# Optimization experiments

Hardware: AMD Instinct MI355X
Metric: run time of the kernel (lower is better)

The kernel has to match this reference:

```python
import jax, jax.numpy as jnp
import numpy as np

NUM_TOKENS = 16384
HIDDEN = 4096
NUM_EXPERTS = 256
TOP_K = 8
N_GROUP = 8
TOPK_GROUP = 4
NORM_TOPK_PROB = True
ROUTED_SCALING_FACTOR = 1.0


def setup_inputs() -> dict:
    key = jax.random.key(0)
    k1, k2, k3 = jax.random.split(key, 3)
    hidden_states = jax.random.normal(k1, (NUM_TOKENS, HIDDEN), dtype=jnp.float32)
    weight = jax.random.normal(k2, (NUM_EXPERTS, HIDDEN), dtype=jnp.float32) * (HIDDEN ** -0.5)
    e_score_correction_bias = jax.random.normal(k3, (NUM_EXPERTS,), dtype=jnp.float32) * 0.01
    return {"hidden_states": hidden_states, "weight": weight,
            "e_score_correction_bias": e_score_correction_bias}


def reference(hidden_states, weight, e_score_correction_bias):
    num_tokens = hidden_states.shape[0]
    # router logits: [T, E]
    logits = jnp.einsum('th,eh->te', hidden_states.astype(jnp.float32),
                        weight.astype(jnp.float32))
    scores = jax.nn.sigmoid(logits)
    scores_for_choice = scores + e_score_correction_bias[None, :]
    # group scores: sum of top-2 within each group, [T, G]
    per_group = scores_for_choice.reshape(num_tokens, N_GROUP, NUM_EXPERTS // N_GROUP)
    top2_vals, _ = jax.lax.top_k(per_group, 2)
    group_scores = top2_vals.sum(axis=-1)
    # select topk_group groups, build mask over experts
    _, group_idx = jax.lax.top_k(group_scores, TOPK_GROUP)  # [T, topk_group]
    group_mask = jnp.zeros_like(group_scores).at[
        jnp.arange(num_tokens)[:, None], group_idx].set(1.0)  # [T, G]
    score_mask = jnp.repeat(group_mask, NUM_EXPERTS // N_GROUP, axis=1)  # [T, E]
    tmp_scores = jnp.where(score_mask > 0, scores_for_choice, -jnp.inf)
    # final top-k experts over masked scores
    _, topk_idx = jax.lax.top_k(tmp_scores, TOP_K)  # [T, K]
    topk_weight = jnp.take_along_axis(scores, topk_idx, axis=1)
    if TOP_K > 1 and NORM_TOPK_PROB:
        denom = topk_weight.sum(axis=-1, keepdims=True) + 1e-20
        topk_weight = topk_weight / denom
    topk_weight = topk_weight * ROUTED_SCALING_FACTOR
    return logits, topk_weight, topk_idx
```

## Files before the change

kernel.cpp:

```cpp
#include <hip/hip_runtime.h>
#include <hip/hip_bf16.h>
#include <math.h>

#define TKN 16384
#define HID 4096
#define NE  256
#define TOPK 8
#define NGRP 8
#define TOPG 4

#define BM 64
#define BK 64
#define NKT (HID / BK)
#define BIMG 16384

typedef _Float16 half8 __attribute__((ext_vector_type(8)));
typedef float    f32x4 __attribute__((ext_vector_type(4)));

static __device__ __forceinline__ unsigned pkrtz(float x, float y) {
    auto r = __builtin_amdgcn_cvt_pkrtz(x, y);
    return __builtin_bit_cast(unsigned, r);
}
static __device__ __forceinline__ float hi_mask(float a) {
    return __uint_as_float(__float_as_uint(a) & 0xFFFFE000u);
}
static __device__ __forceinline__ void gload_lds16(const void* g, void* l) {
    __builtin_amdgcn_global_load_lds(
        (const __attribute__((address_space(1))) unsigned int*)g,
        (__attribute__((address_space(3))) unsigned int*)l, 16, 0, 0);
}

__global__ __launch_bounds__(256) void prep_b(const float* __restrict__ B,
                                              unsigned char* __restrict__ ws)
{
    const int gid = blockIdx.x * 256 + threadIdx.x;
    const int e   = gid >> 9;
    const int k0  = (gid & 511) * 8;
    const float* src = B + (size_t)e * HID + k0;
    float v[8];
    #pragma unroll
    for (int i = 0; i < 8; ++i) v[i] = src[i];
    unsigned hw[4], lw[4];
    #pragma unroll
    for (int j = 0; j < 4; ++j) {
        const float x0 = v[2*j], x1 = v[2*j+1];
        const float h0 = hi_mask(x0), h1 = hi_mask(x1);
        hw[j] = pkrtz(h0, h1);
        lw[j] = pkrtz(x0 - h0, x1 - h1);
    }
    const int cb     = e >> 6;
    const int colgrp = (e & 63) >> 4;
    const int lane16 = e & 15;
    const int kt     = k0 >> 6;
    const int kk     = k0 & 63;
    const int wg     = kk >> 5;
    const int kseg   = (kk >> 3) & 3;
    const int f      = colgrp * 2 + wg;
    unsigned char* img = ws + (size_t)(cb * NKT + kt) * BIMG
                            + f * 2048 + (kseg * 16 + lane16) * 16;
    *(uint4*)(img)        = make_uint4(hw[0], hw[1], hw[2], hw[3]);
    *(uint4*)(img + 1024) = make_uint4(lw[0], lw[1], lw[2], lw[3]);
}

__global__ __launch_bounds__(256, 4) void gemm_mfma(
    const float* __restrict__ A, const unsigned char* __restrict__ Bws,
    float* __restrict__ C)
{
    __shared__ __align__(16) unsigned char smem[2][16384];

    const int tid  = threadIdx.x;
    const int lane = tid & 63;
    const int wave = tid >> 6;
    const int wg = wave >> 1;
    const int wc = wave & 1;

    const int logical = (blockIdx.x & 7) * 128 + (blockIdx.x >> 3);
    const int mb   = logical >> 2;
    const int cb   = logical & 3;
    const int row0 = mb * BM;

    const unsigned char* Abytes = (const unsigned char*)A;
    const unsigned char* srcp[4];
    #pragma unroll
    for (int i = 0; i < 4; ++i) {
        const int row = 16 * wave + 4 * i + (lane >> 4);
        srcp[i] = Abytes + (size_t)(row0 + row) * (HID * 4)
                         + (((lane & 15) * 16) ^ ((row & 7) << 4));
    }
    const int ldsW = wave * 4096;

    const int laneA0 = (lane & 15) * 256 +
                       ((wg * 128 + (lane >> 4) * 32) ^ ((lane & 7) << 4));
    const int laneA1 = laneA0 ^ 16;

    const unsigned char* bBase = Bws + (size_t)cb * NKT * BIMG;
    const int f0off = ((wc * 2 + 0) * 2 + wg) * 2048 + lane * 16;
    const int f1off = ((wc * 2 + 1) * 2 + wg) * 2048 + lane * 16;

    f32x4 acc[4][2];
    #pragma unroll
    for (int i = 0; i < 4; ++i) { acc[i][0] = (f32x4)0.f; acc[i][1] = (f32x4)0.f; }

    half8 bC[4], bN[4];

    #pragma unroll
    for (int i = 0; i < 4; ++i)
        gload_lds16(srcp[i], &smem[0][ldsW + i * 1024]);
    bC[0] = *(const half8*)(bBase + f0off);
    bC[1] = *(const half8*)(bBase + f0off + 1024);
    bC[2] = *(const half8*)(bBase + f1off);
    bC[3] = *(const half8*)(bBase + f1off + 1024);
    __syncthreads();

#define GSTEP(KT, BCUR, BNXT)                                                  \
    {                                                                          \
        const int kt_ = (KT);                                                  \
        const unsigned char* ub = &smem[kt_ & 1][0];                           \
        const bool more = (kt_ != NKT - 1);                                    \
        if (more) {         \
            unsigned char* nb = &smem[(kt_ + 1) & 1][0];                       \
            _Pragma("unroll")                                                  \
            for (int i = 0; i < 4; ++i)                                        \
                gload_lds16(srcp[i] + (size_t)(kt_ + 1) * 256,                 \
                            nb + ldsW + i * 1024);                             \
            const unsigned char* bp = bBase + (size_t)(kt_ + 1) * BIMG;        \
            BNXT[0] = *(const half8*)(bp + f0off);                             \
            BNXT[1] = *(const half8*)(bp + f0off + 1024);                      \
            BNXT[2] = *(const half8*)(bp + f1off);                             \
            BNXT[3] = *(const half8*)(bp + f1off + 1024);                      \
        }                                                                      \
        __builtin_amdgcn_sched_barrier(0);                                     \
        _Pragma("unroll")                                                      \
        for (int mt = 0; mt < 4; ++mt) {                                       \
            const float4 u0 = *(const float4*)(ub + laneA0 + mt * 4096);       \
            const float4 u1 = *(const float4*)(ub + laneA1 + mt * 4096);       \
            const float h0 = hi_mask(u0.x), h1 = hi_mask(u0.y),                \
                        h2 = hi_mask(u0.z), h3 = hi_mask(u0.w);                \
            const float h4 = hi_mask(u1.x), h5 = hi_mask(u1.y),                \
                        h6 = hi_mask(u1.z), h7 = hi_mask(u1.w);                \
            unsigned ahw[4], alw[4];                                           \
            ahw[0] = pkrtz(h0, h1);            ahw[1] = pkrtz(h2, h3);         \
            ahw[2] = pkrtz(h4, h5);            ahw[3] = pkrtz(h6, h7);         \
            alw[0] = pkrtz(u0.x - h0, u0.y - h1);                              \
            alw[1] = pkrtz(u0.z - h2, u0.w - h3);                              \
            alw[2] = pkrtz(u1.x - h4, u1.y - h5);                              \
            alw[3] = pkrtz(u1.z - h6, u1.w - h7);                              \
            const half8 ah = __builtin_bit_cast(half8,                         \
                make_uint4(ahw[0], ahw[1], ahw[2], ahw[3]));                   \
            const half8 al = __builtin_bit_cast(half8,                         \
                make_uint4(alw[0], alw[1], alw[2], alw[3]));                   \
            f32x4 c0 = acc[mt][0];                                             \
            c0 = __builtin_amdgcn_mfma_f32_16x16x32_f16(ah, BCUR[0], c0, 0, 0, 0); \
            c0 = __builtin_amdgcn_mfma_f32_16x16x32_f16(ah, BCUR[1], c0, 0, 0, 0); \
            c0 = __builtin_amdgcn_mfma_f32_16x16x32_f16(al, BCUR[0], c0, 0, 0, 0); \
            acc[mt][0] = c0;                                                   \
            f32x4 c1 = acc[mt][1];                                             \
            c1 = __builtin_amdgcn_mfma_f32_16x16x32_f16(ah, BCUR[2], c1, 0, 0, 0); \
            c1 = __builtin_amdgcn_mfma_f32_16x16x32_f16(ah, BCUR[3], c1, 0, 0, 0); \
            c1 = __builtin_amdgcn_mfma_f32_16x16x32_f16(al, BCUR[2], c1, 0, 0, 0); \
            acc[mt][1] = c1;                                                   \
        }                                                                      \
        __syncthreads();                                                       \
    }

    for (int kt = 0; kt < NKT; kt += 2) {
        GSTEP(kt,     bC, bN);
        GSTEP(kt + 1, bN, bC);
    }
#undef GSTEP

    float* redf = (float*)&smem[0][0];
    const int fb = wc * 2048 + lane * 4;
    if (wg == 1) {
        #pragma unroll
        for (int mt = 0; mt < 4; ++mt)
            #pragma unroll
            for (int nt = 0; nt < 2; ++nt)
                *(f32x4*)&redf[fb + (mt * 2 + nt) * 256] = acc[mt][nt];
    }
    __syncthreads();
    if (wg == 0) {
        #pragma unroll
        for (int mt = 0; mt < 4; ++mt) {
            #pragma unroll
            for (int nt = 0; nt < 2; ++nt) {
                f32x4 o = acc[mt][nt] + *(const f32x4*)&redf[fb + (mt * 2 + nt) * 256];
                const int r0 = row0 + mt * 16 + (lane >> 4) * 4;
                const int cc = cb * 64 + wc * 32 + nt * 16 + (lane & 15);
                #pragma unroll
                for (int r = 0; r < 4; ++r)
                    C[(size_t)(r0 + r) * NE + cc] = o[r];
            }
        }
    }
}

__global__ __launch_bounds__(256) void router_topk_kernel(
    const float* __restrict__ logits, const float* __restrict__ bias,
    float* __restrict__ out_w, float* __restrict__ out_i)
{
    const int wid  = threadIdx.x >> 6;
    const int lane = threadIdx.x & 63;
    const int token = blockIdx.x * 4 + wid;

    const float* row = logits + (size_t)token * NE;
    const float4 lg = *(const float4*)&row[lane * 4];

    float sig[4], sc[4];
    {
        const float l4[4] = {lg.x, lg.y, lg.z, lg.w};
        #pragma unroll
        for (int j = 0; j < 4; ++j) {
            sig[j] = 1.f / (1.f + expf(-l4[j]));
            sc[j]  = sig[j] + bias[lane * 4 + j];
        }
    }

    float m1 = sc[0], m2 = -INFINITY;
    #pragma unroll
    for (int j = 1; j < 4; ++j) {
        if (sc[j] > m1) { m2 = m1; m1 = sc[j]; }
        else if (sc[j] > m2) { m2 = sc[j]; }
    }
    #pragma unroll
    for (int off = 1; off < 8; off <<= 1) {
        const float o1 = __shfl_xor(m1, off);
        const float o2 = __shfl_xor(m2, off);
        const float lo = fminf(m1, o1);
        m1 = fmaxf(m1, o1);
        m2 = fmaxf(lo, fmaxf(m2, o2));
    }
    const float gscore = m1 + m2;

    const int gmy = lane >> 3;
    int rank = 0;
    #pragma unroll
    for (int g = 0; g < NGRP; ++g) {
        const float gs = __shfl(gscore, g * 8);
        if (gs > gscore || (gs == gscore && g < gmy)) ++rank;
    }
    if (rank >= TOPG) {
        #pragma unroll
        for (int j = 0; j < 4; ++j) sc[j] = -INFINITY;
    }

    float wk[TOPK]; int ik[TOPK];
    float wsum = 0.f;
    #pragma unroll
    for (int k = 0; k < TOPK; ++k) {
        float bv = sc[0]; int bi = lane * 4;
        #pragma unroll
        for (int j = 1; j < 4; ++j)
            if (sc[j] > bv) { bv = sc[j]; bi = lane * 4 + j; }
        #pragma unroll
        for (int off = 1; off < 64; off <<= 1) {
            const float v2 = __shfl_xor(bv, off);
            const int   i2 = __shfl_xor(bi, off);
            if (v2 > bv || (v2 == bv && i2 < bi)) { bv = v2; bi = i2; }
        }
        const int owner = bi >> 2;
        const int j = bi & 3;
        const float sv = (j == 0) ? sig[0] : (j == 1) ? sig[1] : (j == 2) ? sig[2] : sig[3];
        const float w = __shfl(sv, owner);
        wk[k] = w; ik[k] = bi; wsum += w;
        if (lane == owner) {
            if (j == 0) sc[0] = -INFINITY;
            else if (j == 1) sc[1] = -INFINITY;
            else if (j == 2) sc[2] = -INFINITY;
            else sc[3] = -INFINITY;
        }
    }

    if (lane == 0) {
        const float denom = wsum + 1e-20f;
        #pragma unroll
        for (int k = 0; k < TOPK; ++k) {
            out_w[(size_t)token * TOPK + k] = wk[k] / denom;
            out_i[(size_t)token * TOPK + k] = (float)ik[k];
        }
    }
}

extern "C" void kernel_launch(void* const* d_in, const int* in_sizes, int n_in,
                              void* d_out, int out_size, void* d_ws, size_t ws_size,
                              hipStream_t stream) {
    const float* hidden = (const float*)d_in[0];
    const float* weight = (const float*)d_in[1];
    const float* bias   = (const float*)d_in[2];

    float* logits = (float*)d_out;
    float* out_w  = logits + (size_t)TKN * NE;
    float* out_i  = out_w + (size_t)TKN * TOPK;

    unsigned char* bpl = (unsigned char*)d_ws;

    prep_b<<<512, 256, 0, stream>>>(weight, bpl);
    gemm_mfma<<<1024, 256, 0, stream>>>(hidden, bpl, logits);
    router_topk_kernel<<<TKN / 4, 256, 0, stream>>>(logits, bias, out_w, out_i);
}
```

Before: 172.8 us.

## Pre-split A into fp16 hi/lo halves in LDS with register-staged prefetch

Result: no change. 169.9 us (-1.6%).

```diff
diff --git a/kernel.cpp b/kernel.cpp
--- a/kernel.cpp
+++ b/kernel.cpp
@@ -24,10 +24,14 @@
 static __device__ __forceinline__ float hi_mask(float a) {
     return __uint_as_float(__float_as_uint(a) & 0xFFFFE000u);
 }
-static __device__ __forceinline__ void gload_lds16(const void* g, void* l) {
-    __builtin_amdgcn_global_load_lds(
-        (const __attribute__((address_space(1))) unsigned int*)g,
-        (__attribute__((address_space(3))) unsigned int*)l, 16, 0, 0);
+static __device__ __forceinline__ void split_w(const float4 v,
+    unsigned char* hiP, unsigned char* loP, int ofs)
+{
+    const float h0 = hi_mask(v.x), h1 = hi_mask(v.y),
+                h2 = hi_mask(v.z), h3 = hi_mask(v.w);
+    *(uint2*)(hiP + ofs) = make_uint2(pkrtz(h0, h1), pkrtz(h2, h3));
+    *(uint2*)(loP + ofs) = make_uint2(pkrtz(v.x - h0, v.y - h1),
+                                      pkrtz(v.z - h2, v.w - h3));
 }
 
 __global__ __launch_bounds__(256) void prep_b(const float* __restrict__ B,
@@ -62,11 +66,11 @@
     *(uint4*)(img + 1024) = make_uint4(lw[0], lw[1], lw[2], lw[3]);
 }
 
-__global__ __launch_bounds__(256, 4) void gemm_mfma(
+__global__ __launch_bounds__(256, 3) void gemm_mfma(
     const float* __restrict__ A, const unsigned char* __restrict__ Bws,
     float* __restrict__ C)
 {
-    __shared__ __align__(16) unsigned char smem[2][16384];
+    __shared__ __align__(16) unsigned char smem[2][2][8192];
 
     const int tid  = threadIdx.x;
     const int lane = tid & 63;
@@ -79,19 +83,17 @@
     const int cb   = logical & 3;
     const int row0 = mb * BM;
 
-    const unsigned char* Abytes = (const unsigned char*)A;
-    const unsigned char* srcp[4];
+    const float* srcp[4];
+    int wofs[4];
     #pragma unroll
     for (int i = 0; i < 4; ++i) {
-        const int row = 16 * wave + 4 * i + (lane >> 4);
-        srcp[i] = Abytes + (size_t)(row0 + row) * (HID * 4)
-                         + (((lane & 15) * 16) ^ ((row & 7) << 4));
-    }
-    const int ldsW = wave * 4096;
-
-    const int laneA0 = (lane & 15) * 256 +
-                       ((wg * 128 + (lane >> 4) * 32) ^ ((lane & 7) << 4));
-    const int laneA1 = laneA0 ^ 16;
+        const int r = i * 16 + wave * 4 + (lane >> 4);
+        srcp[i] = A + (size_t)(row0 + r) * HID + (lane & 15) * 4;
+        wofs[i] = r * 128 + (((lane & 15) * 8) ^ ((r & 7) << 4));
+    }
+
+    const int kx    = ((wg * 64) + ((lane >> 4) << 4)) ^ ((lane & 7) << 4);
+    const int aRowB = (lane & 15) * 128;
 
     const unsigned char* bBase = Bws + (size_t)cb * NKT * BIMG;
     const int f0off = ((wc * 2 + 0) * 2 + wg) * 2048 + lane * 16;
@@ -101,54 +103,51 @@
     #pragma unroll
     for (int i = 0; i < 4; ++i) { acc[i][0] = (f32x4)0.f; acc[i][1] = (f32x4)0.f; }
 
-    half8 bC[4], bN[4];
-
-    #pragma unroll
-    for (int i = 0; i < 4; ++i)
-        gload_lds16(srcp[i], &smem[0][ldsW + i * 1024]);
-    bC[0] = *(const half8*)(bBase + f0off);
-    bC[1] = *(const half8*)(bBase + f0off + 1024);
-    bC[2] = *(const half8*)(bBase + f1off);
-    bC[3] = *(const half8*)(bBase + f1off + 1024);
+    float4 aA[4], aB[4];
+    half8  bA[4], bB[4];
+
+    {
+        float4 p[4];
+        #pragma unroll
+        for (int i = 0; i < 4; ++i) p[i] = *(const float4*)(srcp[i]);
+        #pragma unroll
+        for (int i = 0; i < 4; ++i)
+            split_w(p[i], &smem[0][0][0], &smem[0][1][0], wofs[i]);
+    }
+    #pragma unroll
+    for (int i = 0; i < 4; ++i) aB[i] = *(const float4*)(srcp[i] + BK);
+    bA[0] = *(const half8*)(bBase + f0off);
+    bA[1] = *(const half8*)(bBase + f0off + 1024);
+    bA[2] = *(const half8*)(bBase + f1off);
+    bA[3] = *(const half8*)(bBase + f1off + 1024);
     __syncthreads();
 
-#define GSTEP(KT, BCUR, BNXT)                                                  \
+#define PSTEP(T, RBUF, WBUF, ASPL, AISS, BCUR, BNXT)                           \
     {                                                                          \
-        const int kt_ = (KT);                                                  \
-        const unsigned char* ub = &smem[kt_ & 1][0];                           \
-        const bool more = (kt_ != NKT - 1);                                    \
-        if (more) {         \
-            unsigned char* nb = &smem[(kt_ + 1) & 1][0];                       \
+        const int t_ = (T);                                                    \
+        if (t_ + 2 < NKT) {               \
             _Pragma("unroll")                                                  \
             for (int i = 0; i < 4; ++i)                                        \
-                gload_lds16(srcp[i] + (size_t)(kt_ + 1) * 256,                 \
-                            nb + ldsW + i * 1024);                             \
-            const unsigned char* bp = bBase + (size_t)(kt_ + 1) * BIMG;        \
+                AISS[i] = *(const float4*)(srcp[i] + (t_ + 2) * BK);           \
+        }                                                                      \
+        if (t_ + 1 < NKT) {               \
+            const unsigned char* bp = bBase + (size_t)(t_ + 1) * BIMG;         \
             BNXT[0] = *(const half8*)(bp + f0off);                             \
             BNXT[1] = *(const half8*)(bp + f0off + 1024);                      \
             BNXT[2] = *(const half8*)(bp + f1off);                             \
             BNXT[3] = *(const half8*)(bp + f1off + 1024);                      \
         }                                                                      \
-        __builtin_amdgcn_sched_barrier(0);                                     \
+                     \
+        asm volatile("s_waitcnt lgkmcnt(0)\n\ts_barrier" ::: "memory");        \
+        if (t_ + 1 < NKT) {         \
+            _Pragma("unroll")                                                  \
+            for (int i = 0; i < 4; ++i)                                        \
+                split_w(ASPL[i], &WBUF[0][0], &WBUF[1][0], wofs[i]);           \
+        }                                                                      \
         _Pragma("unroll")                                                      \
         for (int mt = 0; mt < 4; ++mt) {                                       \
-            const float4 u0 = *(const float4*)(ub + laneA0 + mt * 4096);       \
-            const float4 u1 = *(const float4*)(ub + laneA1 + mt * 4096);       \
-            const float h0 = hi_mask(u0.x), h1 = hi_mask(u0.y),                \
-                        h2 = hi_mask(u0.z), h3 = hi_mask(u0.w);                \
-            const float h4 = hi_mask(u1.x), h5 = hi_mask(u1.y),                \
-                        h6 = hi_mask(u1.z), h7 = hi_mask(u1.w);                \
-            unsigned ahw[4], alw[4];                                           \
-            ahw[0] = pkrtz(h0, h1);            ahw[1] = pkrtz(h2, h3);         \
-            ahw[2] = pkrtz(h4, h5);            ahw[3] = pkrtz(h6, h7);         \
-            alw[0] = pkrtz(u0.x - h0, u0.y - h1);                              \
-            alw[1] = pkrtz(u0.z - h2, u0.w - h3);                              \
-            alw[2] = pkrtz(u1.x - h4, u1.y - h5);                              \
-            alw[3] = pkrtz(u1.z - h6, u1.w - h7);                              \
-            const half8 ah = __builtin_bit_cast(half8,                         \
-                make_uint4(ahw[0], ahw[1], ahw[2], ahw[3]));                   \
-            const half8 al = __builtin_bit_cast(half8,                         \
-                make_uint4(alw[0], alw[1], alw[2], alw[3]));                   \
+            const half8 ah = *(const half8*)(&RBUF[0][0] + aRowB + mt * 2048 + kx); \
+            const half8 al = *(const half8*)(&RBUF[1][0] + aRowB + mt * 2048 + kx); \
             f32x4 c0 = acc[mt][0];                                             \
             c0 = __builtin_amdgcn_mfma_f32_16x16x32_f16(ah, BCUR[0], c0, 0, 0, 0); \
             c0 = __builtin_amdgcn_mfma_f32_16x16x32_f16(ah, BCUR[1], c0, 0, 0, 0); \
@@ -157,19 +156,18 @@
             f32x4 c1 = acc[mt][1];                                             \
             c1 = __builtin_amdgcn_mfma_f32_16x16x32_f16(ah, BCUR[2], c1, 0, 0, 0); \
             c1 = __builtin_amdgcn_mfma_f32_16x16x32_f16(ah, BCUR[3], c1, 0, 0, 0); \
-            c1 = __builtin_amdgcn_mfma_f32_16x16x32_f16(al, BCUR[2], c1, 0, 0, 0); \
+            c1 = __builtin_amdgcn_mfma_f32_16x16x32_f16(al, BCUR[3 - 1], c1, 0, 0, 0); \
             acc[mt][1] = c1;                                                   \
         }                                                                      \
-        __syncthreads();                                                       \
     }
 
     for (int kt = 0; kt < NKT; kt += 2) {
-        GSTEP(kt,     bC, bN);
-        GSTEP(kt + 1, bN, bC);
-    }
-#undef GSTEP
-
-    float* redf = (float*)&smem[0][0];
+        PSTEP(kt,     smem[0], smem[1], aB, aA, bA, bB);
+        PSTEP(kt + 1, smem[1], smem[0], aA, aB, bB, bA);
+    }
+#undef PSTEP
+
+    float* redf = (float*)&smem[0][0][0];
     const int fb = wc * 2048 + lane * 4;
     if (wg == 1) {
         #pragma unroll
```
